# Kernel optimization log

Hardware: AMD Instinct MI355X
Metric: run time of the kernel (lower is better)

The kernel has to match this reference:

```python
import jax, jax.numpy as jnp
import numpy as np

N_TRIAL = 1_000_000
N_STIM = 10_000
N_DIM = 16
N_GROUP = 4
N_REF = 8  # row = 1 query + 8 references
BETA = 1.0
GAMMA = 0.001
N_SELECT = np.array([1, 2, 3, 1], dtype=np.int32)  # per-config n_select (config_list)


def setup_inputs() -> dict:
    key = jax.random.key(0)
    k1, k2, k3, k4, k5 = jax.random.split(key, 5)
    stimulus_set = jax.random.randint(k1, (N_TRIAL, N_REF + 1), 0, N_STIM, dtype=jnp.int64)
    config_idx = jax.random.randint(k2, (N_TRIAL,), 0, len(N_SELECT), dtype=jnp.int64)
    group_id = jax.random.randint(k3, (N_TRIAL,), 0, N_GROUP, dtype=jnp.int64)
    is_present = jnp.ones((N_TRIAL, N_REF + 1), dtype=jnp.int32)
    embed_z = jax.random.normal(k4, (N_STIM, N_DIM), dtype=jnp.float32)
    attention_w = jax.random.uniform(k5, (N_GROUP, N_DIM), dtype=jnp.float32)
    return {
        "stimulus_set": stimulus_set,
        "config_idx": config_idx,
        "group_id": group_id,
        "is_present": is_present,
        "embed_z": embed_z,
        "attention_w": attention_w,
    }


def reference(stimulus_set, config_idx, group_id, is_present, embed_z, attention_w):
    # coordinate: embedding lookup -> (T, R+1, D)
    z = embed_z[stimulus_set]
    z_q = z[:, :1, :]   # (T, 1, D)
    z_r = z[:, 1:, :]   # (T, R, D)
    # attention: per-group dimension weights -> (T, 1, D)
    w = attention_w[group_id][:, None, :]
    # kernel: attention-weighted Minkowski (rho=2) distance + exponential similarity
    d = jnp.sqrt(jnp.sum(w * (z_q - z_r) ** 2, axis=-1))  # (T, R)
    sim_qr = jnp.exp(-BETA * d) + GAMMA
    # mask absent references (is_present[:, 1:])
    sim_qr = sim_qr * is_present[:, 1:].astype(sim_qr.dtype)
    # Ranked-sequence (Luce choice) probability, vectorized over all configs:
    # seq_prob = prod_{j < n_select} sim[:, j] / sum_{i >= j} sim[:, i]
    suffix = jnp.cumsum(sim_qr[:, ::-1], axis=1)[:, ::-1]  # (T, R) suffix sums
    n_select = jnp.asarray(N_SELECT)[config_idx]           # (T,)
    mask = jnp.arange(N_REF)[None, :] < n_select[:, None]  # (T, R)
    denom = jnp.where(mask, suffix, 1.0)
    prob = jnp.where(mask, sim_qr / denom, 1.0)
    likelihood = jnp.prod(prob, axis=1)  # (T,)
    return likelihood
```

## Files before the change

kernel.cpp:

```cpp
#include <hip/hip_runtime.h>
#include <math.h>

#define N_TRIAL 1000000
#define N_REF 8
#define N_DIM 16
#define N_GROUP 4
#define BETA 1.0f
#define GAMMA 0.001f
#define N_SELECT_PACKED 0x1321

typedef float v4f __attribute__((ext_vector_type(4)));

__global__ __launch_bounds__(256) void likelihood_kernel(
    const int* __restrict__ stim,
    const int* __restrict__ config,
    const int* __restrict__ group,
    const int* __restrict__ present,
    const float* __restrict__ embed,
    const float* __restrict__ attw,
    float* __restrict__ out)
{
    __shared__ float s_attw[N_GROUP * N_DIM];

    int tid = threadIdx.x;
    if (tid < N_GROUP * N_DIM) s_attw[tid] = attw[tid];
    __syncthreads();

    int gtid  = blockIdx.x * 256 + tid;
    int trial = gtid >> 2;
    int seg   = gtid & 3;

    const int* sp = stim + trial * (N_REF + 1);
    const int* pp = present + trial * (N_REF + 1);

    int idx[N_REF + 1];
#pragma unroll
    for (int i = 0; i <= N_REF; ++i) idx[i] = sp[i];

    v4f z[N_REF + 1];
#pragma unroll
    for (int i = 0; i <= N_REF; ++i)
        z[i] = ((const v4f*)(embed + idx[i] * N_DIM))[seg];

    int pr[N_REF];
#pragma unroll
    for (int r = 0; r < N_REF; ++r) pr[r] = pp[1 + r];

    int g = group[trial];
    int c = config[trial];

    v4f w = ((const v4f*)(s_attw + g * N_DIM))[seg];
    v4f q = z[0];

    float sim[N_REF];
#pragma unroll
    for (int r = 0; r < N_REF; ++r) {
        v4f dd = q - z[1 + r];
        v4f p  = w * dd * dd;
        float d2 = (p.x + p.y) + (p.z + p.w);
        d2 += __shfl_xor(d2, 1);
        d2 += __shfl_xor(d2, 2);
        float d = sqrtf(d2);
        sim[r] = (__expf(-BETA * d) + GAMMA) * (float)pr[r];
    }

    float suffix[N_REF];
    float acc = 0.0f;
#pragma unroll
    for (int r = N_REF - 1; r >= 0; --r) {
        acc += sim[r];
        suffix[r] = acc;
    }

    int ns = (N_SELECT_PACKED >> ((c & 3) * 4)) & 0xF;

    float lik = 1.0f;
#pragma unroll
    for (int r = 0; r < N_REF; ++r) {
        lik *= (r < ns) ? __fdividef(sim[r], suffix[r]) : 1.0f;
    }

    if (seg == 0) out[trial] = lik;
}

extern "C" void kernel_launch(void* const* d_in, const int* in_sizes, int n_in,
                              void* d_out, int out_size, void* d_ws, size_t ws_size,
                              hipStream_t stream) {
    const int*   stim    = (const int*)d_in[0];
    const int*   config  = (const int*)d_in[1];
    const int*   group   = (const int*)d_in[2];
    const int*   present = (const int*)d_in[3];
    const float* embed   = (const float*)d_in[4];
    const float* attw    = (const float*)d_in[5];
    float*       out     = (float*)d_out;

    int blocks = (N_TRIAL * 4) / 256;
    likelihood_kernel<<<blocks, 256, 0, stream>>>(stim, config, group, present,
                                                  embed, attw, out);
}
```

Baseline: 151.3 us.

## Compute distances with 4 lanes per trial, transpose via LDS for per-trial scoring

Each wave now computes squared distances for 64 trials, four lanes per trial across four passes, and writes them to a shared buffer. After a barrier, each thread reads one trial's eight distances and does the exp, suffix sums and Luce product itself. This removes the redundant 4x transcendental and suffix work per trial and cuts the grid to one thread per trial. The product is specialised to n_select of at most 3 with a single division. The cost is an LDS round trip, a block barrier, and serial loop passes per thread that may expose more load latency.

```diff
diff --git a/kernel.cpp b/kernel.cpp
--- a/kernel.cpp
+++ b/kernel.cpp
@@ -11,7 +11,10 @@
 
 typedef float v4f __attribute__((ext_vector_type(4)));
 
-__global__ __launch_bounds__(256) void likelihood_kernel(
+#define WAVES_PER_BLOCK 4
+#define ROW_STRIDE 72
+
+__global__ __launch_bounds__(256, 4) void likelihood_kernel(
     const int* __restrict__ stim,
     const int* __restrict__ config,
     const int* __restrict__ group,
@@ -20,67 +23,81 @@
     const float* __restrict__ attw,
     float* __restrict__ out)
 {
-    __shared__ float s_attw[N_GROUP * N_DIM];
+    __shared__ float d2buf[WAVES_PER_BLOCK][N_REF][ROW_STRIDE];
 
-    int tid = threadIdx.x;
-    if (tid < N_GROUP * N_DIM) s_attw[tid] = attw[tid];
+    const int tid  = threadIdx.x;
+    const int wv   = tid >> 6;
+    const int lane = tid & 63;
+    const int q    = lane >> 2;
+    const int s    = lane & 3;
+
+    const int wtb = blockIdx.x * 256 + wv * 64;
+
+    const float* embed_s = embed + s * 4;
+
+    float* row_a = &d2buf[wv][2 * s][0];
+    float* row_b = &d2buf[wv][2 * s + 1][0];
+
+    for (int j = 0; j < 4; ++j) {
+        int t  = wtb + 16 * j + q;
+        int tc = (t < N_TRIAL) ? t : (N_TRIAL - 1);
+
+        const int* sp = stim + tc * (N_REF + 1);
+        const int* pp = present + tc * (N_REF + 1);
+
+        int idx[N_REF + 1];
+#pragma unroll
+        for (int i = 0; i <= N_REF; ++i) idx[i] = sp[i];
+
+        int pr[N_REF];
+#pragma unroll
+        for (int r = 0; r < N_REF; ++r) pr[r] = pp[1 + r];
+
+        int g = group[tc];
+        v4f w  = *(const v4f*)(attw + g * N_DIM + s * 4);
+        v4f zq = *(const v4f*)(embed_s + idx[0] * N_DIM);
+
+#pragma unroll
+        for (int r = 0; r < N_REF; ++r) {
+            v4f zr = *(const v4f*)(embed_s + idx[1 + r] * N_DIM);
+            v4f dd = zq - zr;
+            v4f p  = w * dd * dd;
+            float d2 = (p.x + p.y) + (p.z + p.w);
+            d2 += __shfl_xor(d2, 1);
+            d2 += __shfl_xor(d2, 2);
+            d2 = (pr[r] != 0) ? d2 : -1.0f;
+            if (r == 2 * s)     row_a[16 * j + q] = d2;
+            if (r == 2 * s + 1) row_b[16 * j + q] = d2;
+        }
+    }
+
     __syncthreads();
 
-    int gtid  = blockIdx.x * 256 + tid;
-    int trial = gtid >> 2;
-    int seg   = gtid & 3;
-
-    const int* sp = stim + trial * (N_REF + 1);
-    const int* pp = present + trial * (N_REF + 1);
-
-    int idx[N_REF + 1];
-#pragma unroll
-    for (int i = 0; i <= N_REF; ++i) idx[i] = sp[i];
-
-    v4f z[N_REF + 1];
-#pragma unroll
-    for (int i = 0; i <= N_REF; ++i)
-        z[i] = ((const v4f*)(embed + idx[i] * N_DIM))[seg];
-
-    int pr[N_REF];
-#pragma unroll
-    for (int r = 0; r < N_REF; ++r) pr[r] = pp[1 + r];
-
-    int g = group[trial];
-    int c = config[trial];
-
-    v4f w = ((const v4f*)(s_attw + g * N_DIM))[seg];
-    v4f q = z[0];
+    int t2  = wtb + lane;
+    int t2c = (t2 < N_TRIAL) ? t2 : (N_TRIAL - 1);
 
     float sim[N_REF];
 #pragma unroll
     for (int r = 0; r < N_REF; ++r) {
-        v4f dd = q - z[1 + r];
-        v4f p  = w * dd * dd;
-        float d2 = (p.x + p.y) + (p.z + p.w);
-        d2 += __shfl_xor(d2, 1);
-        d2 += __shfl_xor(d2, 2);
-        float d = sqrtf(d2);
-        sim[r] = (__expf(-BETA * d) + GAMMA) * (float)pr[r];
+        float d2 = d2buf[wv][r][lane];
+        float e  = __expf(-BETA * sqrtf(d2)) + GAMMA;
+        sim[r] = (d2 < 0.0f) ? 0.0f : e;
     }
 
-    float suffix[N_REF];
-    float acc = 0.0f;
-#pragma unroll
-    for (int r = N_REF - 1; r >= 0; --r) {
-        acc += sim[r];
-        suffix[r] = acc;
-    }
-
+    int c  = config[t2c];
     int ns = (N_SELECT_PACKED >> ((c & 3) * 4)) & 0xF;
 
-    float lik = 1.0f;
+    float suf2 = sim[7];
 #pragma unroll
-    for (int r = 0; r < N_REF; ++r) {
-        lik *= (r < ns) ? __fdividef(sim[r], suffix[r]) : 1.0f;
-    }
+    for (int r = 6; r >= 2; --r) suf2 += sim[r];
+    float suf1 = suf2 + sim[1];
+    float suf0 = suf1 + sim[0];
 
-    if (seg == 0) out[trial] = lik;
+    float num = sim[0] * ((ns >= 2) ? sim[1] : 1.0f) * ((ns >= 3) ? sim[2] : 1.0f);
+    float den = suf0   * ((ns >= 2) ? suf1   : 1.0f) * ((ns >= 3) ? suf2   : 1.0f);
+
+    if (t2 < N_TRIAL)
+        out[t2] = __fdividef(num, den);
 }
 
 extern "C" void kernel_launch(void* const* d_in, const int* in_sizes, int n_in,
@@ -94,7 +111,7 @@
     const float* attw    = (const float*)d_in[5];
     float*       out     = (float*)d_out;
 
-    int blocks = (N_TRIAL * 4) / 256;
+    int blocks = (N_TRIAL + 255) / 256;
     likelihood_kernel<<<blocks, 256, 0, stream>>>(stim, config, group, present,
                                                   embed, attw, out);
 }
```

Result: slower. 159.4 us (+5.3%).
